# Kernel optimization log

Hardware: AMD Instinct MI355X
Metric: run time of the kernel (lower is better)

Reference implementation:

```python
import jax, jax.numpy as jnp
import numpy as np

N = 8192        # total nodes (32 events x 256 hits)
G = 32          # events
K = 15          # knn_graph k
FIN = 4         # n_ftx_in
FOUT = 4        # n_ftx_out
SPACE = 3       # n_ftx_space
LAT = 64        # n_ftx_latent
HID = 2 * LAT   # GIN hidden (n_hidden_nodes)


def _leaky(x):
    return jnp.where(x > 0, x, 0.01 * x)


def setup_inputs() -> dict:
    key = jax.random.key(0)
    ks = jax.random.split(key, 20)

    def p(k, shape, fan_in):
        return (jax.random.normal(k, shape, jnp.float32) / jnp.sqrt(jnp.float32(fan_in)))

    inp = {
        "x": jax.random.normal(ks[0], (N, FIN), jnp.float32),
        "batch": (jnp.arange(N) // (N // G)).astype(jnp.int32),
        "condition": jnp.zeros((G, 1), jnp.float32),
        # space_emb FFN: FIN -> LAT -> LAT
        "W_se1": p(ks[1], (FIN, LAT), FIN), "b_se1": jnp.zeros((LAT,), jnp.float32),
        "W_se2": p(ks[2], (LAT, LAT), LAT), "b_se2": jnp.zeros((LAT,), jnp.float32),
        # GINConv 1 MLP: LAT -> HID -> LAT
        "W_g1a": p(ks[3], (LAT, HID), LAT), "b_g1a": jnp.zeros((HID,), jnp.float32),
        "W_g1b": p(ks[4], (HID, LAT), HID), "b_g1b": jnp.zeros((LAT,), jnp.float32),
        # GINConv 2 MLP
        "W_g2a": p(ks[5], (LAT, HID), LAT), "b_g2a": jnp.zeros((HID,), jnp.float32),
        "W_g2b": p(ks[6], (HID, LAT), HID), "b_g2b": jnp.zeros((LAT,), jnp.float32),
        # out_emb FFN: LAT -> LAT -> FOUT
        "W_oe1": p(ks[7], (LAT, LAT), LAT), "b_oe1": jnp.zeros((LAT,), jnp.float32),
        "W_oe2": p(ks[8], (LAT, FOUT), LAT), "b_oe2": jnp.zeros((FOUT,), jnp.float32),
    }
    return inp


def _knn_graph(pos, batch, k):
    # pairwise squared distances within the same event only; no self-loops
    d = jnp.sum((pos[:, None, :] - pos[None, :, :]) ** 2, axis=-1)  # [N, N]
    ii = jnp.arange(pos.shape[0])
    valid = (batch[:, None] == batch[None, :]) & (ii[:, None] != ii[None, :])
    d = jnp.where(valid, d, jnp.float32(1e30))
    _, nbr = jax.lax.top_k(-d, k)                 # [N, K] nearest neighbor ids
    src = nbr.reshape(-1)                          # neighbor j (source)
    dst = jnp.repeat(ii, k)                        # center i (target)
    return jnp.stack([src, dst])                   # PyG edge_index layout


def _gin(h, src, dst, Wa, ba, Wb, bb):
    # GINConv, eps=0: mlp(x_i + sum_j x_j)
    agg = jax.ops.segment_sum(h[src], dst, num_segments=h.shape[0])
    m = h + agg
    return jnp.maximum(m @ Wa + ba, 0.0) @ Wb + bb


def reference(x, batch, condition,
              W_se1, b_se1, W_se2, b_se2,
              W_g1a, b_g1a, W_g1b, b_g1b,
              W_g2a, b_g2a, W_g2b, b_g2b,
              W_oe1, b_oe1, W_oe2, b_oe2):
    # space_emb FFN
    h = _leaky(x @ W_se1 + b_se1) @ W_se2 + b_se2          # [N, LAT]
    # dynamic knn graph on first SPACE dims of the embedding
    ei = _knn_graph(h[:, :SPACE], batch, K)                 # [2, N*K]
    src, dst = ei[0], ei[1]
    # MPLSeq: 2 GINConv layers with residual skip (cond unused, n_cond=0)
    h = h + _gin(h, src, dst, W_g1a, b_g1a, W_g1b, b_g1b)
    h = h + _gin(h, src, dst, W_g2a, b_g2a, W_g2b, b_g2b)
    # out_emb FFN
    x_emb = _leaky(h @ W_oe1 + b_oe1) @ W_oe2 + b_oe2       # [N, FOUT]
    return (h, x_emb, ei)
```

## Files before the change

kernel.cpp:

```cpp
#include <hip/hip_runtime.h>


#define N_NODES 8192
#define NPE     256
#define KNN     15
#define LAT     64
#define HID     128
#define NK      (N_NODES*KNN)
#define NBLK    512
#define NTHR    512
#define NPB     16
#define NEV     32
#define BPEV    16
#define EI0     (N_NODES*LAT + N_NODES*4)

#define BARA_CNT 0
#define BARA_FLG 4096
#define BARB_CNT 8192
#define BARB_FLG 12288
#define BAR_BYTES 16384

#define OFF_HA  BAR_BYTES
#define OFF_HB  (OFF_HA + N_NODES*LAT*4)
#define OFF_POS (OFF_HB + N_NODES*LAT*4)

typedef unsigned short bf16;
typedef unsigned int   u32;
typedef unsigned long long u64;

__device__ __forceinline__ float bf2f(bf16 s) {
    union { u32 u; float f; } v; v.u = ((u32)s) << 16; return v.f;
}
__device__ __forceinline__ bf16 f2bf(float f) {
    union { float f; u32 u; } v; v.f = f;
    u32 u = v.u + 0x7fffu + ((v.u >> 16) & 1u);
    return (bf16)(u >> 16);
}
__device__ __forceinline__ float ldf(const void* p, int i, int f32) {
    return f32 ? ((const float*)p)[i] : bf2f(((const bf16*)p)[i]);
}
__device__ __forceinline__ void st_coh(float* p, float v) {
    __hip_atomic_store(p, v, __ATOMIC_RELAXED, __HIP_MEMORY_SCOPE_AGENT);
}

struct KArgs {
    const void* x;
    const void* se1; const void* bse1; const void* se2; const void* bse2;
    const void* g1a; const void* bg1a; const void* g1b; const void* bg1b;
    const void* g2a; const void* bg2a; const void* g2b; const void* bg2b;
    const void* oe1; const void* boe1; const void* oe2; const void* boe2;
    const u32* wdet;
    float* hA; float* hB; float* pos; int* bar;
    void* out;
};

struct Shm {
    union {
        int   red[NTHR];
        float hid[NPB][LAT];
        float kpos[NPE * 3];
        struct { float m[NPB*LAT]; float own[NPB*LAT]; float t[NPB*HID]; } g;
        float st[NPB*LAT];
    } u;
    int   snb[NPB*KNN];
    float sh[NPB*LAT];
    int   flag;
};

__device__ __forceinline__ void eventbar(int* cnt, int* flg) {
    asm volatile("s_waitcnt vmcnt(0)" ::: "memory");
    __syncthreads();
    if (threadIdx.x == 0) {
        if (__hip_atomic_fetch_add(cnt, 1, __ATOMIC_RELAXED,
                                   __HIP_MEMORY_SCOPE_AGENT) == BPEV - 1) {
            __hip_atomic_store(flg, 1, __ATOMIC_RELAXED,
                               __HIP_MEMORY_SCOPE_AGENT);
        }
        int guard = 0;
        while (__hip_atomic_load(flg, __ATOMIC_RELAXED,
                                 __HIP_MEMORY_SCOPE_AGENT) == 0) {
            __builtin_amdgcn_s_sleep(2);
            if (++guard > (1 << 20)) break;
        }
        __builtin_amdgcn_fence(__ATOMIC_ACQUIRE, "workgroup");
    }
    __syncthreads();
}

template<bool LAST>
__device__ __forceinline__ void gin_layer(Shm& S, int base, int f32,
        const float* __restrict__ hin, float* hout,
        const void* Wa, const void* ba, const void* Wb, const void* bb,
        void* out)
{
    const int tid = threadIdx.x;
    #pragma unroll
    for (int p = 0; p < 2; p++) {
        const int e = tid + p*NTHR, n = e >> 6, f = e & 63, gi = base + n;
        const int* nb = &S.snb[n*KNN];
        const float own = hin[gi*LAT + f];
        float vv[KNN];
        #pragma unroll
        for (int k = 0; k < KNN; k++) vv[k] = hin[nb[k]*LAT + f];
        float s0 = vv[0] + vv[1],  s1 = vv[2]  + vv[3],  s2 = vv[4]  + vv[5];
        float s3 = vv[6] + vv[7],  s4 = vv[8]  + vv[9],  s5 = vv[10] + vv[11];
        float s6 = vv[12] + vv[13];
        const float acc = own + (((s0 + s1) + (s2 + s3)) + ((s4 + s5) + (s6 + vv[14])));
        S.u.g.m[e] = acc; S.u.g.own[e] = own;
    }
    __syncthreads();
    {
        const int n4 = (tid >> 7) * 4, u = tid & 127;
        float a0 = ldf(ba, u, f32);
        float a1 = a0, a2 = a0, a3 = a0;
        if (f32) {
            const float* W = (const float*)Wa;
            #pragma unroll 8
            for (int f = 0; f < LAT; f++) {
                const float w = W[f*HID + u];
                a0 = fmaf(S.u.g.m[(n4    )*LAT + f], w, a0);
                a1 = fmaf(S.u.g.m[(n4 + 1)*LAT + f], w, a1);
                a2 = fmaf(S.u.g.m[(n4 + 2)*LAT + f], w, a2);
                a3 = fmaf(S.u.g.m[(n4 + 3)*LAT + f], w, a3);
            }
        } else {
            const bf16* W = (const bf16*)Wa;
            #pragma unroll 8
            for (int f = 0; f < LAT; f++) {
                const float w = bf2f(W[f*HID + u]);
                a0 = fmaf(S.u.g.m[(n4    )*LAT + f], w, a0);
                a1 = fmaf(S.u.g.m[(n4 + 1)*LAT + f], w, a1);
                a2 = fmaf(S.u.g.m[(n4 + 2)*LAT + f], w, a2);
                a3 = fmaf(S.u.g.m[(n4 + 3)*LAT + f], w, a3);
            }
        }
        S.u.g.t[(n4    )*HID + u] = a0 > 0.f ? a0 : 0.f;
        S.u.g.t[(n4 + 1)*HID + u] = a1 > 0.f ? a1 : 0.f;
        S.u.g.t[(n4 + 2)*HID + u] = a2 > 0.f ? a2 : 0.f;
        S.u.g.t[(n4 + 3)*HID + u] = a3 > 0.f ? a3 : 0.f;
    }
    __syncthreads();
    {
        const int q = tid >> 6, f = tid & 63;
        float a0 = ldf(bb, f, f32);
        float a1 = a0;
        if (f32) {
            const float* W = (const float*)Wb;
            #pragma unroll 8
            for (int u = 0; u < HID; u++) {
                const float w = W[u*LAT + f];
                a0 = fmaf(S.u.g.t[(q    )*HID + u], w, a0);
                a1 = fmaf(S.u.g.t[(q + 8)*HID + u], w, a1);
            }
        } else {
            const bf16* W = (const bf16*)Wb;
            #pragma unroll 8
            for (int u = 0; u < HID; u++) {
                const float w = bf2f(W[u*LAT + f]);
                a0 = fmaf(S.u.g.t[(q    )*HID + u], w, a0);
                a1 = fmaf(S.u.g.t[(q + 8)*HID + u], w, a1);
            }
        }
        const float o0 = S.u.g.own[(q    )*LAT + f] + a0;
        const float o1 = S.u.g.own[(q + 8)*LAT + f] + a1;
        const int gi0 = base + q, gi1 = base + q + 8;
        if (!LAST) {
            st_coh(&hout[gi0*LAT + f], o0);
            st_coh(&hout[gi1*LAT + f], o1);
        } else {
            S.sh[(q    )*LAT + f] = o0;
            S.sh[(q + 8)*LAT + f] = o1;
            if (f32) {
                ((float*)out)[gi0*LAT + f] = o0;
                ((float*)out)[gi1*LAT + f] = o1;
            } else {
                ((bf16*)out)[gi0*LAT + f] = f2bf(o0);
                ((bf16*)out)[gi1*LAT + f] = f2bf(o1);
            }
        }
    }
    __syncthreads();
}

__global__ __launch_bounds__(NTHR, 4) void k_fused(KArgs a)
{
    __shared__ Shm S;
    const int tid = threadIdx.x, blk = blockIdx.x;
    const int ev   = blk & (NEV - 1);
    const int slc  = blk >> 5;
    const int base = ev * NPE + slc * NPB;

    {
        int c = 0;
        for (int i = tid; i < 4096; i += NTHR) {
            const u32 x = a.wdet[i];
            c += ((x >> 7)  & 0xffu) >= 0xC8u;
            c += ((x >> 23) & 0xffu) >= 0xC8u;
        }
        S.u.red[tid] = c;
        __syncthreads();
        for (int s = NTHR/2; s > 0; s >>= 1) {
            if (tid < s) S.u.red[tid] += S.u.red[tid + s];
            __syncthreads();
        }
        if (tid == 0) S.flag = (S.u.red[0] > 64) ? 1 : 0;
        __syncthreads();
    }
    const int f32 = S.flag;
    __syncthreads();

    {
        #pragma unroll
        for (int p = 0; p < 2; p++) {
            const int e = tid + p*NTHR, n = e >> 6, f = e & 63, node = base + n;
            float acc = ldf(a.bse1, f, f32);
            #pragma unroll
            for (int i = 0; i < 4; i++)
                acc = fmaf(ldf(a.x, node*4 + i, f32), ldf(a.se1, i*LAT + f, f32), acc);
            acc = acc > 0.f ? acc : 0.01f*acc;
            S.u.hid[n][f] = acc;
        }
        __syncthreads();
        const int q = tid >> 6, f = tid & 63;
        float a0 = ldf(a.bse2, f, f32);
        float a1 = a0;
        if (f32) {
            const float* W = (const float*)a.se2;
            #pragma unroll 8
            for (int j = 0; j < LAT; j++) {
                const float w = W[j*LAT + f];
                a0 = fmaf(S.u.hid[q][j],     w, a0);
                a1 = fmaf(S.u.hid[q + 8][j], w, a1);
            }
        } else {
            const bf16* W = (const bf16*)a.se2;
            #pragma unroll 8
            for (int j = 0; j < LAT; j++) {
                const float w = bf2f(W[j*LAT + f]);
                a0 = fmaf(S.u.hid[q][j],     w, a0);
                a1 = fmaf(S.u.hid[q + 8][j], w, a1);
            }
        }
        const int n0 = base + q, n1 = base + q + 8;
        st_coh(&a.hA[n0*LAT + f], a0);
        st_coh(&a.hA[n1*LAT + f], a1);
        if (f < 3) {
            st_coh(&a.pos[n0*3 + f], a0);
            st_coh(&a.pos[n1*3 + f], a1);
        }
    }
    eventbar(a.bar + (BARA_CNT + ev*128)/4, a.bar + (BARA_FLG + ev*128)/4);

    {
        const int eb = ev * NPE;
        for (int i = tid; i < NPE*3; i += NTHR) S.u.kpos[i] = a.pos[(size_t)eb*3 + i];
        __syncthreads();
        const int wave = tid >> 6, lane = tid & 63;
        #pragma unroll
        for (int t = 0; t < 2; ++t) {
            const int n  = base + wave*2 + t;
            const int nl = n - eb;
            const float px = S.u.kpos[nl*3], py = S.u.kpos[nl*3+1], pz = S.u.kpos[nl*3+2];
            u64 key[4];
            #pragma unroll
            for (int c = 0; c < 4; c++) {
                const int j = 64*c + lane;
                const float dx = px - S.u.kpos[j*3], dy = py - S.u.kpos[j*3+1],
                            dz = pz - S.u.kpos[j*3+2];
                float dd = __fmul_rn(dx, dx);
                dd = __fadd_rn(dd, __fmul_rn(dy, dy));
                dd = __fadd_rn(dd, __fmul_rn(dz, dz));
                key[c] = ((u64)__float_as_uint(dd) << 32) | (u32)j;
                if (j == nl) key[c] = ~0ull;
            }
            #define CSWAP(A,B) { const u64 x_ = key[A], y_ = key[B]; \
                                 key[A] = x_ < y_ ? x_ : y_; key[B] = x_ < y_ ? y_ : x_; }
            CSWAP(0,1) CSWAP(2,3) CSWAP(0,2) CSWAP(1,3) CSWAP(1,2)
            #undef CSWAP
            int myj = 0;
            #pragma unroll
            for (int k = 0; k < KNN; k++) {
                u64 m = key[0];
                #pragma unroll
                for (int s = 32; s >= 1; s >>= 1) {
                    const u64 o = __shfl_xor(m, s, 64);
                    m = o < m ? o : m;
                }
                if (lane == k) myj = (int)(u32)m;
                const bool hit = (key[0] == m);
                key[0] = hit ? key[1] : key[0];
                key[1] = hit ? key[2] : key[1];
                key[2] = hit ? key[3] : key[2];
                key[3] = hit ? ~0ull  : key[3];
            }
            if (lane < KNN) {
                const int gj = eb + myj;
                S.snb[(n - base)*KNN + lane] = gj;
                if (f32) {
                    float* o = (float*)a.out;
                    o[EI0 + n*KNN + lane]      = (float)gj;
                    o[EI0 + NK + n*KNN + lane] = (float)n;
                } else {
                    bf16* o = (bf16*)a.out;
                    o[EI0 + n*KNN + lane]      = f2bf((float)gj);
                    o[EI0 + NK + n*KNN + lane] = f2bf((float)n);
                }
            }
        }
        __syncthreads();
    }

    gin_layer<false>(S, base, f32, a.hA, a.hB,
                     a.g1a, a.bg1a, a.g1b, a.bg1b, nullptr);
    eventbar(a.bar + (BARB_CNT + ev*128)/4, a.bar + (BARB_FLG + ev*128)/4);

    gin_layer<true>(S, base, f32, a.hB, nullptr,
                    a.g2a, a.bg2a, a.g2b, a.bg2b, a.out);

    {
        const int q = tid >> 6, f = tid & 63;
        float a0 = ldf(a.boe1, f, f32);
        float a1 = a0;
        if (f32) {
            const float* W = (const float*)a.oe1;
            #pragma unroll 8
            for (int j = 0; j < LAT; j++) {
                const float w = W[j*LAT + f];
                a0 = fmaf(S.sh[(q    )*LAT + j], w, a0);
                a1 = fmaf(S.sh[(q + 8)*LAT + j], w, a1);
            }
        } else {
            const bf16* W = (const bf16*)a.oe1;
            #pragma unroll 8
            for (int j = 0; j < LAT; j++) {
                const float w = bf2f(W[j*LAT + f]);
                a0 = fmaf(S.sh[(q    )*LAT + j], w, a0);
                a1 = fmaf(S.sh[(q + 8)*LAT + j], w, a1);
            }
        }
        a0 = a0 > 0.f ? a0 : 0.01f*a0;
        a1 = a1 > 0.f ? a1 : 0.01f*a1;
        __syncthreads();
        S.u.st[(q    )*LAT + f] = a0;
        S.u.st[(q + 8)*LAT + f] = a1;
        __syncthreads();
        if (tid < NPB*4) {
            const int n = tid >> 2, ff = tid & 3;
            float acc = ldf(a.boe2, ff, f32);
            for (int j = 0; j < LAT; j++)
                acc = fmaf(S.u.st[n*LAT + j], ldf(a.oe2, j*4 + ff, f32), acc);
            const int xo = N_NODES*LAT + (base + n)*4 + ff;
            if (f32) ((float*)a.out)[xo] = acc;
            else     ((bf16*)a.out)[xo] = f2bf(acc);
        }
    }
}

extern "C" void kernel_launch(void* const* d_in, const int* in_sizes, int n_in,
                              void* d_out, int out_size, void* d_ws, size_t ws_size,
                              hipStream_t stream)
{
    (void)in_sizes; (void)n_in; (void)out_size; (void)ws_size;
    char* ws = (char*)d_ws;

    KArgs a;
    a.x   = d_in[0];
    a.se1 = d_in[3];  a.bse1 = d_in[4];  a.se2 = d_in[5];  a.bse2 = d_in[6];
    a.g1a = d_in[7];  a.bg1a = d_in[8];  a.g1b = d_in[9];  a.bg1b = d_in[10];
    a.g2a = d_in[11]; a.bg2a = d_in[12]; a.g2b = d_in[13]; a.bg2b = d_in[14];
    a.oe1 = d_in[15]; a.boe1 = d_in[16]; a.oe2 = d_in[17]; a.boe2 = d_in[18];
    a.wdet = (const u32*)d_in[7];
    a.hA  = (float*)(ws + OFF_HA);
    a.hB  = (float*)(ws + OFF_HB);
    a.pos = (float*)(ws + OFF_POS);
    a.bar = (int*)ws;
    a.out = d_out;

    hipMemsetAsync(d_ws, 0, BAR_BYTES, stream);
    k_fused<<<dim3(NBLK), dim3(NTHR), 0, stream>>>(a);
}
```

Before: 146.7 us.

## Use split-bf16 MFMA for GIN MLPs and vectorize neighbor aggregation

Replaces the scalar FMA loops of both GIN MLP matmuls with 16x16x32 bf16 MFMA instructions. To keep accuracy close to fp32, operands are split into hi/lo bf16 parts and three MFMAs are issued per tile. The neighbor aggregation now uses float4 loads split across two thread halves with a shared-memory reduction, and the knn positions move to a structure-of-arrays layout to avoid strided LDS access. This adds conversion overhead, more shared memory (padded buffers no longer in the union, which may lower occupancy), and a small precision risk from the bf16 split.

Measured after the change: 132.6 us. 9.6% less time.

```diff
diff --git a/kernel.cpp b/kernel.cpp
--- a/kernel.cpp
+++ b/kernel.cpp
@@ -13,6 +13,8 @@
 #define NEV     32
 #define BPEV    16
 #define EI0     (N_NODES*LAT + N_NODES*4)
+#define PADM    68
+#define PADT    136
 
 #define BARA_CNT 0
 #define BARA_FLG 4096
@@ -27,6 +29,8 @@
 typedef unsigned short bf16;
 typedef unsigned int   u32;
 typedef unsigned long long u64;
+typedef short s16x8 __attribute__((ext_vector_type(8)));
+typedef float f32x4 __attribute__((ext_vector_type(4)));
 
 __device__ __forceinline__ float bf2f(bf16 s) {
     union { u32 u; float f; } v; v.u = ((u32)s) << 16; return v.f;
@@ -41,6 +45,44 @@
 }
 __device__ __forceinline__ void st_coh(float* p, float v) {
     __hip_atomic_store(p, v, __ATOMIC_RELAXED, __HIP_MEMORY_SCOPE_AGENT);
+}
+
+union Frag { u32 w[4]; s16x8 v; };
+
+__device__ __forceinline__ u32 cvtpk(float a, float b) {
+    u32 r; asm("v_cvt_pk_bf16_f32 %0, %1, %2" : "=v"(r) : "v"(a), "v"(b));
+    return r;
+}
+__device__ __forceinline__ float lo2f(u32 w) { union {u32 u; float f;} v; v.u = w << 16;          return v.f; }
+__device__ __forceinline__ float hi2f(u32 w) { union {u32 u; float f;} v; v.u = w & 0xffff0000u;  return v.f; }
+
+__device__ __forceinline__ void split8(const float* x, Frag& hi, Frag& lo) {
+    #pragma unroll
+    for (int i = 0; i < 4; i++) {
+        hi.w[i] = cvtpk(x[2*i], x[2*i+1]);
+        lo.w[i] = cvtpk(x[2*i]   - lo2f(hi.w[i]),
+                        x[2*i+1] - hi2f(hi.w[i]));
+    }
+}
+__device__ __forceinline__ void packA(const float* p, Frag& hi, Frag& lo) {
+    float xv[8];
+    *(float4*)&xv[0] = *(const float4*)p;
+    *(float4*)&xv[4] = *(const float4*)(p + 4);
+    split8(xv, hi, lo);
+}
+__device__ __forceinline__ void loadB_bf(const bf16* p, int stride, Frag& f) {
+    #pragma unroll
+    for (int i = 0; i < 4; i++)
+        f.w[i] = (u32)p[(2*i)*stride] | ((u32)p[(2*i+1)*stride] << 16);
+}
+__device__ __forceinline__ void loadB_f32(const float* p, int stride, Frag& hi, Frag& lo) {
+    float xv[8];
+    #pragma unroll
+    for (int j = 0; j < 8; j++) xv[j] = p[j*stride];
+    split8(xv, hi, lo);
+}
+__device__ __forceinline__ f32x4 MF(const Frag& a, const Frag& b, f32x4 c) {
+    return __builtin_amdgcn_mfma_f32_16x16x32_bf16(a.v, b.v, c, 0, 0, 0);
 }
 
 struct KArgs {
@@ -56,14 +98,17 @@
 
 struct Shm {
     union {
-        int   red[NTHR];
-        float hid[NPB][LAT];
-        float kpos[NPE * 3];
-        struct { float m[NPB*LAT]; float own[NPB*LAT]; float t[NPB*HID]; } g;
-        float st[NPB*LAT];
+        int    red[NTHR];
+        float  hid[NPB][LAT];
+        struct { float x[NPE], y[NPE], z[NPE]; } k;
+        float4 part[2][NPB][16];
+        float  st[NPB*LAT];
     } u;
+    float m[NPB*PADM];
+    float own[NPB*LAT];
+    struct { bf16 hi[NPB*PADT]; bf16 lo[NPB*PADT]; } t;
+    float sh[NPB*LAT];
     int   snb[NPB*KNN];
-    float sh[NPB*LAT];
     int   flag;
 };
 
@@ -94,88 +139,106 @@
         void* out)
 {
     const int tid = threadIdx.x;
-    #pragma unroll
-    for (int p = 0; p < 2; p++) {
-        const int e = tid + p*NTHR, n = e >> 6, f = e & 63, gi = base + n;
+    const int lane = tid & 63, wv = tid >> 6;
+    const int ln15 = lane & 15, kg = lane >> 4;
+
+    {
+        const int h = tid >> 8, n = (tid >> 4) & 15, slot = tid & 15;
+        const float4* h4 = (const float4*)hin;
         const int* nb = &S.snb[n*KNN];
-        const float own = hin[gi*LAT + f];
-        float vv[KNN];
-        #pragma unroll
-        for (int k = 0; k < KNN; k++) vv[k] = hin[nb[k]*LAT + f];
-        float s0 = vv[0] + vv[1],  s1 = vv[2]  + vv[3],  s2 = vv[4]  + vv[5];
-        float s3 = vv[6] + vv[7],  s4 = vv[8]  + vv[9],  s5 = vv[10] + vv[11];
-        float s6 = vv[12] + vv[13];
-        const float acc = own + (((s0 + s1) + (s2 + s3)) + ((s4 + s5) + (s6 + vv[14])));
-        S.u.g.m[e] = acc; S.u.g.own[e] = own;
-    }
-    __syncthreads();
-    {
-        const int n4 = (tid >> 7) * 4, u = tid & 127;
-        float a0 = ldf(ba, u, f32);
-        float a1 = a0, a2 = a0, a3 = a0;
+        float4 s4;
+        if (h == 0) {
+            s4 = h4[(size_t)(base + n)*16 + slot];
+            *(float4*)&S.own[n*LAT + slot*4] = s4;
+            #pragma unroll
+            for (int k = 0; k < 7; k++) {
+                const float4 v = h4[(size_t)nb[k]*16 + slot];
+                s4.x += v.x; s4.y += v.y; s4.z += v.z; s4.w += v.w;
+            }
+        } else {
+            s4 = h4[(size_t)nb[7]*16 + slot];
+            #pragma unroll
+            for (int k = 8; k < 15; k++) {
+                const float4 v = h4[(size_t)nb[k]*16 + slot];
+                s4.x += v.x; s4.y += v.y; s4.z += v.z; s4.w += v.w;
+            }
+        }
+        S.u.part[h][n][slot] = s4;
+        __syncthreads();
+        if (tid < 256) {
+            const int n2 = tid >> 4, sl = tid & 15;
+            const float4 p0 = S.u.part[0][n2][sl], p1 = S.u.part[1][n2][sl];
+            float4 mm; mm.x = p0.x + p1.x; mm.y = p0.y + p1.y;
+            mm.z = p0.z + p1.z; mm.w = p0.w + p1.w;
+            *(float4*)&S.m[n2*PADM + sl*4] = mm;
+        }
+        __syncthreads();
+    }
+
+    {
+        const int u0 = wv * 16;
+        const float bias = ldf(ba, u0 + ln15, f32);
+        f32x4 acc; acc[0] = bias; acc[1] = bias; acc[2] = bias; acc[3] = bias;
+        Frag a0h, a0l, a1h, a1l;
+        packA(&S.m[ln15*PADM +  0 + kg*8], a0h, a0l);
+        packA(&S.m[ln15*PADM + 32 + kg*8], a1h, a1l);
         if (f32) {
             const float* W = (const float*)Wa;
-            #pragma unroll 8
-            for (int f = 0; f < LAT; f++) {
-                const float w = W[f*HID + u];
-                a0 = fmaf(S.u.g.m[(n4    )*LAT + f], w, a0);
-                a1 = fmaf(S.u.g.m[(n4 + 1)*LAT + f], w, a1);
-                a2 = fmaf(S.u.g.m[(n4 + 2)*LAT + f], w, a2);
-                a3 = fmaf(S.u.g.m[(n4 + 3)*LAT + f], w, a3);
-            }
+            Frag b0h, b0l, b1h, b1l;
+            loadB_f32(W + ( 0 + kg*8)*HID + u0 + ln15, HID, b0h, b0l);
+            loadB_f32(W + (32 + kg*8)*HID + u0 + ln15, HID, b1h, b1l);
+            acc = MF(a0h, b0h, acc); acc = MF(a0l, b0h, acc); acc = MF(a0h, b0l, acc);
+            acc = MF(a1h, b1h, acc); acc = MF(a1l, b1h, acc); acc = MF(a1h, b1l, acc);
         } else {
             const bf16* W = (const bf16*)Wa;
-            #pragma unroll 8
-            for (int f = 0; f < LAT; f++) {
-                const float w = bf2f(W[f*HID + u]);
-                a0 = fmaf(S.u.g.m[(n4    )*LAT + f], w, a0);
-                a1 = fmaf(S.u.g.m[(n4 + 1)*LAT + f], w, a1);
-                a2 = fmaf(S.u.g.m[(n4 + 2)*LAT + f], w, a2);
-                a3 = fmaf(S.u.g.m[(n4 + 3)*LAT + f], w, a3);
-            }
-        }
-        S.u.g.t[(n4    )*HID + u] = a0 > 0.f ? a0 : 0.f;
-        S.u.g.t[(n4 + 1)*HID + u] = a1 > 0.f ? a1 : 0.f;
-        S.u.g.t[(n4 + 2)*HID + u] = a2 > 0.f ? a2 : 0.f;
-        S.u.g.t[(n4 + 3)*HID + u] = a3 > 0.f ? a3 : 0.f;
+            Frag b0, b1;
+            loadB_bf(W + ( 0 + kg*8)*HID + u0 + ln15, HID, b0);
+            loadB_bf(W + (32 + kg*8)*HID + u0 + ln15, HID, b1);
+            acc = MF(a0h, b0, acc); acc = MF(a0l, b0, acc);
+            acc = MF(a1h, b1, acc); acc = MF(a1l, b1, acc);
+        }
+        #pragma unroll
+        for (int r = 0; r < 4; r++) {
+            const int row = kg*4 + r;
+            float v = acc[r]; v = v > 0.f ? v : 0.f;
+            const bf16 h = f2bf(v);
+            S.t.hi[row*PADT + u0 + ln15] = h;
+            S.t.lo[row*PADT + u0 + ln15] = f2bf(v - bf2f(h));
+        }
     }
     __syncthreads();
-    {
-        const int q = tid >> 6, f = tid & 63;
-        float a0 = ldf(bb, f, f32);
-        float a1 = a0;
-        if (f32) {
-            const float* W = (const float*)Wb;
-            #pragma unroll 8
-            for (int u = 0; u < HID; u++) {
-                const float w = W[u*LAT + f];
-                a0 = fmaf(S.u.g.t[(q    )*HID + u], w, a0);
-                a1 = fmaf(S.u.g.t[(q + 8)*HID + u], w, a1);
-            }
-        } else {
-            const bf16* W = (const bf16*)Wb;
-            #pragma unroll 8
-            for (int u = 0; u < HID; u++) {
-                const float w = bf2f(W[u*LAT + f]);
-                a0 = fmaf(S.u.g.t[(q    )*HID + u], w, a0);
-                a1 = fmaf(S.u.g.t[(q + 8)*HID + u], w, a1);
-            }
-        }
-        const float o0 = S.u.g.own[(q    )*LAT + f] + a0;
-        const float o1 = S.u.g.own[(q + 8)*LAT + f] + a1;
-        const int gi0 = base + q, gi1 = base + q + 8;
-        if (!LAST) {
-            st_coh(&hout[gi0*LAT + f], o0);
-            st_coh(&hout[gi1*LAT + f], o1);
-        } else {
-            S.sh[(q    )*LAT + f] = o0;
-            S.sh[(q + 8)*LAT + f] = o1;
+
+    if (wv < 4) {
+        const int f0 = wv * 16;
+        const float bias = ldf(bb, f0 + ln15, f32);
+        f32x4 acc; acc[0] = bias; acc[1] = bias; acc[2] = bias; acc[3] = bias;
+        #pragma unroll
+        for (int s = 0; s < 4; s++) {
+            Frag ah, al;
+            ah.v = *(const s16x8*)&S.t.hi[ln15*PADT + s*32 + kg*8];
+            al.v = *(const s16x8*)&S.t.lo[ln15*PADT + s*32 + kg*8];
             if (f32) {
-                ((float*)out)[gi0*LAT + f] = o0;
-                ((float*)out)[gi1*LAT + f] = o1;
+                const float* W = (const float*)Wb;
+                Frag bh, bl;
+                loadB_f32(W + (s*32 + kg*8)*LAT + f0 + ln15, LAT, bh, bl);
+                acc = MF(ah, bh, acc); acc = MF(al, bh, acc); acc = MF(ah, bl, acc);
             } else {
-                ((bf16*)out)[gi0*LAT + f] = f2bf(o0);
-                ((bf16*)out)[gi1*LAT + f] = f2bf(o1);
+                const bf16* W = (const bf16*)Wb;
+                Frag b;
+                loadB_bf(W + (s*32 + kg*8)*LAT + f0 + ln15, LAT, b);
+                acc = MF(ah, b, acc); acc = MF(al, b, acc);
+            }
+        }
+        #pragma unroll
+        for (int r = 0; r < 4; r++) {
+            const int row = kg*4 + r, f = f0 + ln15, gi = base + row;
+            const float o = acc[r] + S.own[row*LAT + f];
+            if (!LAST) {
+                st_coh(&hout[gi*LAT + f], o);
+            } else {
+                S.sh[row*LAT + f] = o;
+                if (f32) ((float*)out)[gi*LAT + f] = o;
+                else     ((bf16*)out)[gi*LAT + f] = f2bf(o);
             }
         }
     }
@@ -253,20 +316,24 @@
 
     {
         const int eb = ev * NPE;
-        for (int i = tid; i < NPE*3; i += NTHR) S.u.kpos[i] = a.pos[(size_t)eb*3 + i];
+        if (tid < NPE) {
+            S.u.k.x[tid] = a.pos[(size_t)(eb + tid)*3 + 0];
+            S.u.k.y[tid] = a.pos[(size_t)(eb + tid)*3 + 1];
+            S.u.k.z[tid] = a.pos[(size_t)(eb + tid)*3 + 2];
+        }
         __syncthreads();
         const int wave = tid >> 6, lane = tid & 63;
         #pragma unroll
         for (int t = 0; t < 2; ++t) {
             const int n  = base + wave*2 + t;
             const int nl = n - eb;
-            const float px = S.u.kpos[nl*3], py = S.u.kpos[nl*3+1], pz = S.u.kpos[nl*3+2];
+            const float px = S.u.k.x[nl], py = S.u.k.y[nl], pz = S.u.k.z[nl];
             u64 key[4];
             #pragma unroll
             for (int c = 0; c < 4; c++) {
                 const int j = 64*c + lane;
-                const float dx = px - S.u.kpos[j*3], dy = py - S.u.kpos[j*3+1],
-                            dz = pz - S.u.kpos[j*3+2];
+                const float dx = px - S.u.k.x[j], dy = py - S.u.k.y[j],
+                            dz = pz - S.u.k.z[j];
                 float dd = __fmul_rn(dx, dx);
                 dd = __fadd_rn(dd, __fmul_rn(dy, dy));
                 dd = __fadd_rn(dd, __fmul_rn(dz, dz));
```
